# Kernel tuning notes

Measured on AMD Instinct MI355X. Metric: run time of the kernel, lower is better.

Reference implementation:

```python
import jax, jax.numpy as jnp
import numpy as np

LAYER_NUM = 2
NUM_CLS = 128
HIDDEN = 256
NUM_NODES = 1024


def setup_inputs() -> dict:
    key = jax.random.key(0)
    ks = jax.random.split(key, 12)
    s = 0.05
    return {
        "x": jax.random.normal(ks[0], (NUM_NODES, HIDDEN), jnp.float32),
        "knowledge": jax.random.uniform(ks[1], (NUM_CLS, NUM_CLS), jnp.float32) / NUM_CLS,
        "w3w": jax.random.normal(ks[2], (HIDDEN, 2 * HIDDEN), jnp.float32) * s,
        "b3w": jax.random.normal(ks[3], (HIDDEN,), jnp.float32) * s,
        "u3": jax.random.normal(ks[4], (HIDDEN, HIDDEN), jnp.float32) * s,
        "bu3": jax.random.normal(ks[5], (HIDDEN,), jnp.float32) * s,
        "w4w": jax.random.normal(ks[6], (HIDDEN, 2 * HIDDEN), jnp.float32) * s,
        "b4w": jax.random.normal(ks[7], (HIDDEN,), jnp.float32) * s,
        "w5w": jax.random.normal(ks[8], (HIDDEN, 2 * HIDDEN), jnp.float32) * s,
        "b5w": jax.random.normal(ks[9], (HIDDEN,), jnp.float32) * s,
        "u5": jax.random.normal(ks[10], (HIDDEN, HIDDEN), jnp.float32) * s,
        "bu5": jax.random.normal(ks[11], (HIDDEN,), jnp.float32) * s,
    }


def reference(x, knowledge, w3w, b3w, u3, bu3, w4w, b4w, w5w, b5w, u5, bu5):
    N, H = x.shape
    C = knowledge.shape[0]
    # hidden[n, c, :] = x[n, :]  (repeat per class)
    hidden = jnp.broadcast_to(x[:, None, :], (N, C, H))
    for _ in range(LAYER_NUM):
        hs = hidden.sum(0)                      # [C, H]
        diff = hs[None, :, :] - hidden          # [N, C, H]
        # knowledge.T @ diff_n  and  knowledge @ diff_n, vectorized over nodes
        left = jnp.einsum('kc,nkh->nch', knowledge, diff)
        right = jnp.einsum('ck,nkh->nch', knowledge, diff)
        av = jnp.concatenate([left, right], axis=-1).reshape(N * C, 2 * H)
        h = hidden.reshape(N * C, H)
        uh3 = h @ u3.T + bu3                    # shared: rv uses fc_eq3_u (source quirk)
        zv = jax.nn.sigmoid(av @ w3w.T + b3w + uh3)
        rv = jax.nn.sigmoid(av @ w4w.T + b4w + uh3)
        hv = jnp.tanh(av @ w5w.T + b5w + (rv * h) @ u5.T + bu5)
        h = (1.0 - zv) * h + zv * hv
        hidden = h.reshape(N, C, H)
    return hidden
```

## Files before the change

kernel.cpp:

```cpp
#include <hip/hip_runtime.h>
#include <cstdint>
#include <cstddef>


#define NODES 1024
#define NCLS  128
#define HID   256

using frag  = __attribute__((ext_vector_type(8))) short;
using frag4 = __attribute__((ext_vector_type(4))) short;
using f32x4 = __attribute__((ext_vector_type(4))) float;

__device__ __forceinline__ float bf2f(unsigned short h){
  unsigned int u = ((unsigned int)h) << 16;
  float f; __builtin_memcpy(&f, &u, 4); return f;
}
__device__ __forceinline__ unsigned short f2bf(float f){
  unsigned int u; __builtin_memcpy(&u, &f, 4);
  u = (u + 0x7fffu + ((u >> 16) & 1u)) >> 16;
  return (unsigned short)u;
}
__device__ __forceinline__ float sigm(float x){ return 1.0f/(1.0f + __expf(-x)); }
__device__ __forceinline__ float tanh_fast(float x){ return 1.0f - 2.0f/(__expf(2.0f*x) + 1.0f); }

#define GLOBAL_AS(p) ((const __attribute__((address_space(1))) void*)(p))
#define LDS_AS(p)    ((__attribute__((address_space(3))) void*)(p))
#define MFMA16 __builtin_amdgcn_mfma_f32_16x16x32_bf16

template<int OUT_BF16>
__global__ __launch_bounds__(256) void gemm_bf16(
    const unsigned short* __restrict__ A0, int ldA0, int K0,
    const unsigned short* __restrict__ A1, int ldA1,
    const unsigned short* __restrict__ BT, int ldB, long bStride,
    void* __restrict__ Cptr, int ldC,
    int Ntiles, int Ktot, unsigned int aMask, int Mtiles)
{
  __shared__ unsigned short As[4096];
  __shared__ unsigned short Bs[4096];
  const int t   = threadIdx.x;
  const int bid = blockIdx.x;
  const int xcd = bid & 7, slot = bid >> 3;
  const int mtPerX = (Mtiles >= 8) ? (Mtiles >> 3) : 1;
  const int mt = xcd * mtPerX + slot / Ntiles;
  const int nt = slot % Ntiles;
  const int lane = t & 63, w = t >> 6;
  const int wm = w >> 1, wn = w & 1;
  const int r = lane & 15, q = lane >> 4;
  const int m0 = mt * 128, n0 = nt * 128;
  const unsigned short* Bbase = BT + (size_t)mt * (size_t)bStride;

  f32x4 acc[4][4] = {};

  for (int kb = 0; kb < Ktot; kb += 32) {
#pragma unroll
    for (int i = 0; i < 2; ++i) {
      int u  = i * 256 + t;
      int mi = u >> 2;
      int kc = (u & 3) * 8;
      int k  = kb + kc;
      const unsigned short* ga;
      if (k < K0) ga = A0 + (size_t)((unsigned int)(m0 + mi) & aMask) * (size_t)ldA0 + k;
      else        ga = A1 + (size_t)(m0 + mi) * (size_t)ldA1 + (k - K0);
      __builtin_amdgcn_global_load_lds(GLOBAL_AS(ga), LDS_AS(&As[u * 8]), 16, 0, 0);
      const unsigned short* gb = Bbase + (size_t)(n0 + mi) * (size_t)ldB + k;
      __builtin_amdgcn_global_load_lds(GLOBAL_AS(gb), LDS_AS(&Bs[u * 8]), 16, 0, 0);
    }
    __syncthreads();

    frag af[4], bf_[4];
#pragma unroll
    for (int x = 0; x < 4; ++x) {
      af[x]  = *(const frag*)&As[(wm * 64 + x * 16 + r) * 32 + q * 8];
      bf_[x] = *(const frag*)&Bs[(wn * 64 + x * 16 + r) * 32 + q * 8];
    }
#pragma unroll
    for (int x = 0; x < 4; ++x)
#pragma unroll
      for (int y = 0; y < 4; ++y)
        acc[x][y] = MFMA16(af[x], bf_[y], acc[x][y], 0, 0, 0);
    __syncthreads();
  }

#pragma unroll
  for (int x = 0; x < 4; ++x) {
#pragma unroll
    for (int y = 0; y < 4; ++y) {
      int col = n0 + wn * 64 + y * 16 + r;
#pragma unroll
      for (int g = 0; g < 4; ++g) {
        long row = m0 + wm * 64 + x * 16 + q * 4 + g;
        if (OUT_BF16) ((unsigned short*)Cptr)[row * (long)ldC + col] = f2bf(acc[x][y][g]);
        else          ((float*)Cptr)[row * (long)ldC + col] = acc[x][y][g];
      }
    }
  }
}

__global__ __launch_bounds__(512, 2) void gemm_pre(
    const unsigned short* __restrict__ AVH, const unsigned short* __restrict__ H1,
    const unsigned short* __restrict__ WB, const float* __restrict__ SG,
    unsigned short* __restrict__ PRE)
{
  __shared__ __align__(16) unsigned short SM[65536];
  const int t   = threadIdx.x;
  const int bid = blockIdx.x;
  const int xcd = bid & 7, slot = bid >> 3;
  const int mt = xcd * 64 + slot / 3;
  const int ct = slot % 3;
  const int lane = t & 63, w = t >> 6;
  const int wm = w >> 2, wn = w & 3;
  const int r = lane & 15, q = lane >> 4;
  const int m0 = mt * 256;
  const unsigned short* Wrow = WB + (size_t)(ct * 256) * 768;
  const int nkt = (ct < 2) ? 12 : 8;

  unsigned short* const Ab0 = SM;
  unsigned short* const Ab1 = SM + 16384;
  unsigned short* const Bb0 = SM + 32768;
  unsigned short* const Bb1 = SM + 49152;

  f32x4 acc[8][4] = {};

  const int smi = t >> 3, sc = t & 7;

  auto ISSUE_A = [&](unsigned short* dst, int kt, int rbase) {
    int row = rbase + smi;
    int gc = sc ^ (row & 7);
    const unsigned short* ga;
    if (kt < 8) ga = AVH + (size_t)(m0 + row) * 512 + kt * 64 + gc * 8;
    else        ga = H1  + (size_t)(m0 + row) * 256 + (kt - 8) * 64 + gc * 8;
    __builtin_amdgcn_global_load_lds(GLOBAL_AS(ga), LDS_AS(&dst[row * 64 + sc * 8]), 16, 0, 0);
  };
  auto ISSUE_B = [&](unsigned short* dst, int kt, int rbase) {
    int row = rbase + smi;
    int gc = sc ^ (row & 7);
    __builtin_amdgcn_global_load_lds(GLOBAL_AS(Wrow + (size_t)row * 768 + kt * 64 + gc * 8),
                                     LDS_AS(&dst[row * 64 + sc * 8]), 16, 0, 0);
  };

  ISSUE_B(Bb0, 0, 0); ISSUE_B(Bb0, 0, 64); ISSUE_B(Bb0, 0, 128); ISSUE_B(Bb0, 0, 192);
  ISSUE_A(Ab0, 0, 0); ISSUE_A(Ab0, 0, 128); ISSUE_A(Ab0, 0, 64); ISSUE_A(Ab0, 0, 192);
  asm volatile("s_waitcnt vmcnt(2)" ::: "memory");
  __builtin_amdgcn_s_barrier();

#define PRE_PHASE(XG0, ISSUES, TAIL)                                         \
    {                                                                        \
      int ra0 = wm * 128 + (XG0) * 16 + r, ra1 = ra0 + 16;                   \
      frag a00 = *(const frag*)&A[ra0 * 64 + ((q ^ (ra0 & 7)) * 8)];         \
      frag a01 = *(const frag*)&A[ra0 * 64 + (((4 + q) ^ (ra0 & 7)) * 8)];   \
      frag a10 = *(const frag*)&A[ra1 * 64 + ((q ^ (ra1 & 7)) * 8)];         \
      frag a11 = *(const frag*)&A[ra1 * 64 + (((4 + q) ^ (ra1 & 7)) * 8)];   \
      ISSUES;                                                                \
      __builtin_amdgcn_s_setprio(1);                                         \
      _Pragma("unroll")                                                      \
      for (int y = 0; y < 4; ++y) {                                          \
        acc[(XG0)][y]     = MFMA16(a00, bf[y][0], acc[(XG0)][y], 0, 0, 0);   \
        acc[(XG0)][y]     = MFMA16(a01, bf[y][1], acc[(XG0)][y], 0, 0, 0);   \
        acc[(XG0)+1][y]   = MFMA16(a10, bf[y][0], acc[(XG0)+1][y], 0, 0, 0); \
        acc[(XG0)+1][y]   = MFMA16(a11, bf[y][1], acc[(XG0)+1][y], 0, 0, 0); \
      }                                                                      \
      __builtin_amdgcn_s_setprio(0);                                         \
      TAIL;                                                                  \
      asm volatile("" ::: "memory");                                         \
      __builtin_amdgcn_s_barrier();                                          \
    }

  for (int kt = 0; kt < nkt; ++kt) {
    unsigned short* A  = (kt & 1) ? Ab1 : Ab0;
    unsigned short* B  = (kt & 1) ? Bb1 : Bb0;
    unsigned short* An = (kt & 1) ? Ab0 : Ab1;
    unsigned short* Bn = (kt & 1) ? Bb0 : Bb1;
    const bool more = (kt + 1 < nkt);

    frag bf[4][2];
#pragma unroll
    for (int y = 0; y < 4; ++y) {
      int rb = wn * 64 + y * 16 + r;
      bf[y][0] = *(const frag*)&B[rb * 64 + ((q ^ (rb & 7)) * 8)];
      bf[y][1] = *(const frag*)&B[rb * 64 + (((4 + q) ^ (rb & 7)) * 8)];
    }

    PRE_PHASE(0,
      { if (more) { ISSUE_B(Bn, kt + 1, 0); ISSUE_B(Bn, kt + 1, 64); } },
      { })
    PRE_PHASE(2,
      { if (more) { ISSUE_B(Bn, kt + 1, 128); ISSUE_B(Bn, kt + 1, 192); } },
      { if (more) asm volatile("s_waitcnt vmcnt(4)" ::: "memory");
        else      asm volatile("s_waitcnt vmcnt(0)" ::: "memory"); })
    PRE_PHASE(4,
      { if (more) { ISSUE_A(An, kt + 1, 0); ISSUE_A(An, kt + 1, 128); } },
      { })
    PRE_PHASE(6,
      { if (more) { ISSUE_A(An, kt + 1, 64); ISSUE_A(An, kt + 1, 192); } },
      { if (more) asm volatile("s_waitcnt vmcnt(2)" ::: "memory"); })
  }
#undef PRE_PHASE

  unsigned short* L = SM;
#pragma unroll
  for (int xg = 0; xg < 8; ++xg) {
#pragma unroll
    for (int y = 0; y < 4; ++y) {
      int j = wn * 64 + y * 16 + r;
      int jc = j >> 3, jl = j & 7;
#pragma unroll
      for (int g = 0; g < 4; ++g) {
        int c = wm * 128 + xg * 16 + q * 4 + g;
        L[c * 256 + ((jc ^ (c & 31)) * 8) + jl] = f2bf(acc[xg][y][g]);
      }
    }
  }
  __syncthreads();
  if (ct == 1) {
#pragma unroll
    for (int rr = 0; rr < 16; ++rr) {
      int unit = rr * 512 + t;
      int row = unit >> 5, ch = unit & 31;
      size_t grow = (size_t)(m0 + row);
      frag v  = *(const frag*)&L[row * 256 + ((ch ^ (row & 31)) * 8)];
      frag hh = *(const frag*)(H1 + grow * 256 + ch * 8);
      const float* sgr = SG + (size_t)(row & 127) * 768 + 256 + ch * 8;
      f32x4 s0 = *(const f32x4*)(sgr);
      f32x4 s1 = *(const f32x4*)(sgr + 4);
      frag o;
#pragma unroll
      for (int e = 0; e < 8; ++e) {
        float sv = (e < 4) ? s0[e] : s1[e - 4];
        float rv = sigm(sv + bf2f((unsigned short)v[e]));
        o[e] = (short)f2bf(rv * bf2f((unsigned short)hh[e]));
      }
      *(frag*)&PRE[grow * 768 + 256 + ch * 8] = o;
    }
  } else {
#pragma unroll
    for (int rr = 0; rr < 16; ++rr) {
      int unit = rr * 512 + t;
      int row = unit >> 5, ch = unit & 31;
      frag v = *(const frag*)&L[row * 256 + ((ch ^ (row & 31)) * 8)];
      *(frag*)&PRE[(size_t)(m0 + row) * 768 + ct * 256 + ch * 8] = v;
    }
  }
}

__global__ __launch_bounds__(256, 2) void gemm_l1(
    const float* __restrict__ XW, const float* __restrict__ SW,
    const float* __restrict__ x,
    const float* __restrict__ b3, const float* __restrict__ b4,
    const float* __restrict__ b5, const float* __restrict__ bu3,
    const float* __restrict__ bu5,
    const float* __restrict__ colsum, const float* __restrict__ rowsum,
    const unsigned short* __restrict__ u5b,
    const unsigned short* __restrict__ KTbN, const unsigned short* __restrict__ KbN,
    unsigned short* __restrict__ H1, unsigned short* __restrict__ AVH)
{
  __shared__ unsigned short SM[17408];
  unsigned short* As = SM;
  unsigned short* Bs = SM + 4096;
  unsigned short* L  = SM;
  __shared__ float tP1[256], tP2[256], tP3[256], tX[256];
  __shared__ float tZ1[256], tZ2[256], tZ3[256];
  __shared__ float tV1[256], tV2[256], tV3[256];
  __shared__ float tCS[128], tRS[128];

  const int t = threadIdx.x, bid = blockIdx.x;
  const int xcd = bid & 7, slot = bid >> 3;
  const int n  = xcd * 128 + (slot >> 1);
  const int nt = slot & 1;
  const int lane = t & 63, w = t >> 6, wm = w >> 1, wn = w & 1;
  const int r = lane & 15, q = lane >> 4;
  const int n0 = nt * 128;
  const float* xw = XW + (size_t)n * 1792;

  {
    int i = t;
    float xwi0 = xw[i], xwi1 = xw[256 + i], xwi2 = xw[512 + i], xwi3 = xw[768 + i];
    float xwi4 = xw[1024 + i], xwi5 = xw[1280 + i], xwu = xw[1536 + i];
    tP1[i] = SW[512 + i] - xwi2;
    tP2[i] = SW[768 + i] - xwi3;
    tP3[i] = xwu + b4[i] + bu3[i];
    tX[i]  = x[(size_t)n * HID + i];
    tZ1[i] = SW[i] - xwi0;
    tZ2[i] = SW[256 + i] - xwi1;
    tZ3[i] = xwu + b3[i] + bu3[i];
    tV1[i] = SW[1024 + i] - xwi4;
    tV2[i] = SW[1280 + i] - xwi5;
    tV3[i] = b5[i] + bu5[i];
    if (t < 128) { tCS[t] = colsum[t]; tRS[t] = rowsum[t]; }
  }
  __syncthreads();

  f32x4 acc[4][4] = {};

  for (int kb = 0; kb < 256; kb += 32) {
#pragma unroll
    for (int i = 0; i < 2; ++i) {
      int u  = i * 256 + t;
      int mi = u >> 2;
      int c  = u & 3;
      int k  = kb + c * 8;
      int gc = c ^ ((mi >> 1) & 3);
      __builtin_amdgcn_global_load_lds(GLOBAL_AS(u5b + (size_t)(n0 + mi) * 256 + kb + gc * 8),
                                       LDS_AS(&Bs[u * 8]), 16, 0, 0);
      float cs = tCS[mi], rs = tRS[mi];
      frag a;
#pragma unroll
      for (int e = 0; e < 8; ++e) {
        int i2 = k + e;
        float pre = cs * tP1[i2] + rs * tP2[i2] + tP3[i2];
        a[e] = (short)f2bf(sigm(pre) * tX[i2]);
      }
      *(frag*)&As[mi * 32 + (gc * 8)] = a;
    }
    __syncthreads();

    frag af[4], bf_[4];
#pragma unroll
    for (int xx = 0; xx < 4; ++xx) {
      int ra = wm * 64 + xx * 16 + r;
      int rb = wn * 64 + xx * 16 + r;
      af[xx]  = *(const frag*)&As[ra * 32 + ((q ^ ((ra >> 1) & 3)) * 8)];
      bf_[xx] = *(const frag*)&Bs[rb * 32 + ((q ^ ((rb >> 1) & 3)) * 8)];
    }
#pragma unroll
    for (int xx = 0; xx < 4; ++xx)
#pragma unroll
      for (int y = 0; y < 4; ++y)
        acc[xx][y] = MFMA16(af[xx], bf_[y], acc[xx][y], 0, 0, 0);
    __syncthreads();
  }

#pragma unroll
  for (int xx = 0; xx < 4; ++xx) {
#pragma unroll
    for (int y = 0; y < 4; ++y) {
      int j = wn * 64 + y * 16 + r;
      int i = n0 + j;
      frag4 pack;
#pragma unroll
      for (int g = 0; g < 4; ++g) {
        int c = wm * 64 + xx * 16 + q * 4 + g;
        float cs = tCS[c], rs = tRS[c];
        float z  = sigm(cs * tZ1[i] + rs * tZ2[i] + tZ3[i]);
        float p5 = cs * tV1[i] + rs * tV2[i] + tV3[i] + acc[xx][y][g];
        float h1 = (1.0f - z) * tX[i] + z * tanh_fast(p5);
        unsigned short hb = f2bf(h1);
        pack[g] = (short)hb;
        H1[(size_t)(n * 128 + c) * HID + i] = hb;
      }
      *(frag4*)&L[j * 136 + (wm * 64 + xx * 16 + q * 4)] = pack;
    }
  }
  __syncthreads();

#pragma unroll 1
  for (int s = 0; s < 2; ++s) {
    const unsigned short* Ks = s ? KbN : KTbN;
#pragma unroll
    for (int xx = 0; xx < 4; ++xx)
#pragma unroll
      for (int y = 0; y < 4; ++y)
        acc[xx][y] = (f32x4){0.0f, 0.0f, 0.0f, 0.0f};
#pragma unroll
    for (int kb = 0; kb < 4; ++kb) {
      frag af[4], bf_[4];
#pragma unroll
      for (int xx = 0; xx < 4; ++xx) {
        int cp = wm * 64 + xx * 16 + r;
        af[xx] = *(const frag*)(Ks + (size_t)cp * 128 + kb * 32 + q * 8);
        int j = wn * 64 + xx * 16 + r;
        bf_[xx] = *(const frag*)&L[j * 136 + kb * 32 + q * 8];
      }
#pragma unroll
      for (int xx = 0; xx < 4; ++xx)
#pragma unroll
        for (int y = 0; y < 4; ++y)
          acc[xx][y] = MFMA16(af[xx], bf_[y], acc[xx][y], 0, 0, 0);
    }
#pragma unroll
    for (int xx = 0; xx < 4; ++xx)
#pragma unroll
      for (int y = 0; y < 4; ++y) {
        int col = s * 256 + n0 + wn * 64 + y * 16 + r;
#pragma unroll
        for (int g = 0; g < 4; ++g) {
          int cp = wm * 64 + xx * 16 + q * 4 + g;
          AVH[(size_t)(n * 128 + cp) * 512 + col] = f2bf(acc[xx][y][g]);
        }
      }
  }
}

__global__ __launch_bounds__(256, 3) void gemm_l2(
    const unsigned short* __restrict__ PRE, const float* __restrict__ SG,
    const unsigned short* __restrict__ H1, const unsigned short* __restrict__ u5b,
    float* __restrict__ out)
{
  __shared__ __align__(16) unsigned short SM[16384];
  unsigned short* const As = SM;
  unsigned short* const Bs = SM + 4096;
  float* L = (float*)SM;

  const int t = threadIdx.x, bid = blockIdx.x;
  const int xcd = bid & 7, slot = bid >> 3;
  const int mt = xcd * 128 + (slot >> 1);
  const int nt = slot & 1;
  const int lane = t & 63, w = t >> 6, wm = w >> 1, wn = w & 1;
  const int r = lane & 15, q = lane >> 4;
  const int m0 = mt * 128, n0 = nt * 128;

  f32x4 acc[4][4] = {};

  for (int kb = 0; kb < 256; kb += 32) {
#pragma unroll
    for (int i = 0; i < 2; ++i) {
      int u  = i * 256 + t;
      int mi = u >> 2;
      int gc = (u & 3) ^ ((mi >> 1) & 3);
      __builtin_amdgcn_global_load_lds(GLOBAL_AS(PRE + (size_t)(m0 + mi) * 768 + 256 + kb + gc * 8),
                                       LDS_AS(&As[u * 8]), 16, 0, 0);
      __builtin_amdgcn_global_load_lds(GLOBAL_AS(u5b + (size_t)(n0 + mi) * 256 + kb + gc * 8),
                                       LDS_AS(&Bs[u * 8]), 16, 0, 0);
    }
    __syncthreads();

    frag af[4], bf_[4];
#pragma unroll
    for (int xx = 0; xx < 4; ++xx) {
      int ra = wm * 64 + xx * 16 + r;
      int rb = wn * 64 + xx * 16 + r;
      af[xx]  = *(const frag*)&As[ra * 32 + ((q ^ ((ra >> 1) & 3)) * 8)];
      bf_[xx] = *(const frag*)&Bs[rb * 32 + ((q ^ ((rb >> 1) & 3)) * 8)];
    }
#pragma unroll
    for (int xx = 0; xx < 4; ++xx)
#pragma unroll
      for (int y = 0; y < 4; ++y)
        acc[xx][y] = MFMA16(af[xx], bf_[y], acc[xx][y], 0, 0, 0);
    __syncthreads();
  }

  const int lr_r = t >> 2;
  const int cb   = t & 3;
#pragma unroll 1
  for (int p = 0; p < 2; ++p) {
    if (p) __syncthreads();
    if (wm == p) {
#pragma unroll
      for (int xx = 0; xx < 4; ++xx)
#pragma unroll
        for (int y = 0; y < 4; ++y) {
          int j = wn * 64 + y * 16 + r;
#pragma unroll
          for (int g = 0; g < 4; ++g) {
            int lr = xx * 16 + q * 4 + g;
            L[lr * 128 + (j ^ ((lr & 7) << 2))] = acc[xx][y][g];
          }
        }
    }
    __syncthreads();
    long grow = m0 + p * 64 + lr_r;
    int cc = (int)(grow & 127);
    const unsigned short* prow = PRE + (size_t)grow * 768;
    const unsigned short* hrow = H1 + (size_t)grow * 256;
    const float* sgr = SG + (size_t)cc * 768;
    const int off = (lr_r & 7) << 2;
#pragma unroll
    for (int gi = 0; gi < 4; ++gi) {
      int j0 = cb * 8 + gi * 32;
      int i0 = n0 + j0;
      f32x4 a0 = *(const f32x4*)&L[lr_r * 128 + (j0 ^ off)];
      f32x4 a1 = *(const f32x4*)&L[lr_r * 128 + ((j0 + 4) ^ off)];
      frag pz = *(const frag*)(prow + i0);
      frag pp = *(const frag*)(prow + 512 + i0);
      frag hh = *(const frag*)(hrow + i0);
      f32x4 sz0 = *(const f32x4*)(sgr + i0);
      f32x4 sz1 = *(const f32x4*)(sgr + i0 + 4);
      f32x4 sp0 = *(const f32x4*)(sgr + 512 + i0);
      f32x4 sp1 = *(const f32x4*)(sgr + 512 + i0 + 4);
      f32x4 o0, o1;
#pragma unroll
      for (int e = 0; e < 8; ++e) {
        float sz = (e < 4) ? sz0[e] : sz1[e - 4];
        float sp = (e < 4) ? sp0[e] : sp1[e - 4];
        float av = (e < 4) ? a0[e] : a1[e - 4];
        float z  = sigm(sz + bf2f((unsigned short)pz[e]));
        float pv = sp + bf2f((unsigned short)pp[e]) + av;
        float h  = bf2f((unsigned short)hh[e]);
        float o  = (1.0f - z) * h + z * tanh_fast(pv);
        if (e < 4) o0[e] = o; else o1[e - 4] = o;
      }
      *(f32x4*)&out[(size_t)grow * 256 + i0] = o0;
      *(f32x4*)&out[(size_t)grow * 256 + i0 + 4] = o1;
    }
  }
}

__global__ __launch_bounds__(256) void prep_cast(
    const float* __restrict__ x, const float* __restrict__ Kn,
    const float* __restrict__ w3, const float* __restrict__ u3,
    const float* __restrict__ w4, const float* __restrict__ w5,
    const float* __restrict__ u5,
    unsigned short* __restrict__ xb, unsigned short* __restrict__ WB,
    unsigned short* __restrict__ WB2, unsigned short* __restrict__ u5b,
    unsigned short* __restrict__ KbN, unsigned short* __restrict__ KTbN)
{
  int idx = blockIdx.x * 256 + threadIdx.x;
  if (idx < 262144) { xb[idx] = f2bf(x[idx]); return; }
  idx -= 262144;
  if (idx < 589824) {
    int col = idx / 768, j = idx % 768;
    int g = col >> 8, i = col & 255;
    float v;
    if (j < 512) { const float* wg = (g == 0) ? w3 : (g == 1) ? w4 : w5; v = wg[(size_t)i * 512 + j]; }
    else v = (g < 2) ? u3[(size_t)i * 256 + (j - 512)] : 0.0f;
    WB[(size_t)col * 768 + j] = f2bf(v);
    return;
  }
  idx -= 589824;
  if (idx < 458752) {
    int col = idx / 256, h = idx % 256;
    int b = col >> 8, i = col & 255;
    float v = (b < 6) ? ((b < 2 ? w3 : (b < 4 ? w4 : w5))[(size_t)i * 512 + (b & 1) * 256 + h])
                      : u3[(size_t)i * 256 + h];
    WB2[(size_t)col * 256 + h] = f2bf(v);
    return;
  }
  idx -= 458752;
  if (idx < 65536) { u5b[idx] = f2bf(u5[idx]); return; }
  idx -= 65536;
  if (idx < 16384) { int c = idx >> 7, k = idx & 127; KbN[idx]  = f2bf(-Kn[c * 128 + k]); return; }
  idx -= 16384;
  { int c = idx >> 7, k = idx & 127; KTbN[idx] = f2bf(-Kn[k * 128 + c]); }
}

__global__ __launch_bounds__(256) void prep_reduce(
    const float* __restrict__ x, const float* __restrict__ Kn,
    float* __restrict__ S, float* __restrict__ colsum, float* __restrict__ rowsum)
{
  int b = blockIdx.x, t = threadIdx.x;
  if (b < 8) {
    float s = 0.f;
    for (int n = 0; n < 128; ++n) s += x[(size_t)(b * 128 + n) * HID + t];
    atomicAdd(&S[t], s);
  } else if (b == 8) {
    if (t < NCLS) { float s = 0.f; for (int k = 0; k < NCLS; ++k) s += Kn[k * NCLS + t]; colsum[t] = s; }
  } else {
    if (t < NCLS) { float s = 0.f; for (int k = 0; k < NCLS; ++k) s += Kn[t * NCLS + k]; rowsum[t] = s; }
  }
}

__global__ __launch_bounds__(256) void prep_sw(
    const float* __restrict__ S, const float* __restrict__ w3,
    const float* __restrict__ w4, const float* __restrict__ w5, float* __restrict__ SW)
{
  int col = blockIdx.x * 256 + threadIdx.x;
  int b = col >> 8, i = col & 255;
  const float* w = (b < 2) ? w3 : (b < 4) ? w4 : w5;
  const float* row = w + (size_t)i * 512 + (b & 1) * 256;
  float s = 0.f;
  for (int h = 0; h < HID; ++h) s += S[h] * row[h];
  SW[col] = s;
}

__global__ __launch_bounds__(256) void reduce_hs(
    const unsigned short* __restrict__ H1, float* __restrict__ hs)
{
  int bid = blockIdx.x;
  int c = bid >> 5, nch = bid & 31;
  int i = threadIdx.x;
  const unsigned short* p = H1 + (size_t)nch * 32 * NCLS * HID + (size_t)c * HID + i;
  float s = 0.f;
  for (int n = 0; n < 32; ++n) s += bf2f(p[(size_t)n * NCLS * HID]);
  atomicAdd(&hs[c * HID + i], s);
}

__global__ __launch_bounds__(256) void p2a(
    const float* __restrict__ hs, const float* __restrict__ w3,
    const float* __restrict__ w4, const float* __restrict__ w5, float* __restrict__ hsW)
{
  __shared__ float hrow[HID];
  int k = blockIdx.x & 127, b = blockIdx.x >> 7;
  int t = threadIdx.x;
  hrow[t] = hs[k * HID + t];
  __syncthreads();
  const float* w = (b < 2) ? w3 : (b < 4) ? w4 : w5;
  const float* row = w + (size_t)t * 512 + (b & 1) * 256;
  float s = 0.f;
  for (int h = 0; h < HID; ++h) s += hrow[h] * row[h];
  hsW[(size_t)k * 1536 + b * 256 + t] = s;
}

__global__ __launch_bounds__(256) void p2b(
    const float* __restrict__ hsW, const float* __restrict__ Kn,
    const float* __restrict__ b3, const float* __restrict__ b4, const float* __restrict__ b5,
    const float* __restrict__ bu3, const float* __restrict__ bu5, float* __restrict__ SG)
{
  __shared__ float kc[NCLS], kr[NCLS];
  int c = blockIdx.x, t = threadIdx.x;
  if (t < NCLS) { kc[t] = Kn[t * NCLS + c]; kr[t] = Kn[c * NCLS + t]; }
  __syncthreads();
  for (int g = 0; g < 3; ++g) {
    int i = t;
    const float* L = hsW + (size_t)(2 * g) * 256 + i;
    const float* R = hsW + (size_t)(2 * g + 1) * 256 + i;
    float s = 0.f;
    for (int k = 0; k < NCLS; ++k) s += kc[k] * L[(size_t)k * 1536] + kr[k] * R[(size_t)k * 1536];
    const float* bg = (g == 0) ? b3 : (g == 1) ? b4 : b5;
    s += bg[i] + ((g < 2) ? bu3[i] : bu5[i]);
    SG[(size_t)c * 768 + g * 256 + i] = s;
  }
}

extern "C" void kernel_launch(void* const* d_in, const int* in_sizes, int n_in,
                              void* d_out, int out_size, void* d_ws, size_t ws_size,
                              hipStream_t stream) {
  (void)in_sizes; (void)n_in; (void)out_size; (void)ws_size;
  const float* x   = (const float*)d_in[0];
  const float* Kn  = (const float*)d_in[1];
  const float* w3  = (const float*)d_in[2];
  const float* b3  = (const float*)d_in[3];
  const float* u3  = (const float*)d_in[4];
  const float* bu3 = (const float*)d_in[5];
  const float* w4  = (const float*)d_in[6];
  const float* b4  = (const float*)d_in[7];
  const float* w5  = (const float*)d_in[8];
  const float* b5  = (const float*)d_in[9];
  const float* u5  = (const float*)d_in[10];
  const float* bu5 = (const float*)d_in[11];
  float* out = (float*)d_out;

  char* w = (char*)d_ws;
  unsigned short* AVH = (unsigned short*)(w);
  unsigned short* PRE = (unsigned short*)(w + 134217728);
  unsigned short* H1  = (unsigned short*)(w + 335544320);
  float*          XW  = (float*)(w + 402653184);
  char* misc = w + 409993216;
  float* S      = (float*)(misc);
  float* hs     = (float*)(misc + 1024);
  float* SW     = (float*)(misc + 132096);
  float* colsum = (float*)(misc + 138240);
  float* rowsum = (float*)(misc + 138752);
  float* hsW    = (float*)(misc + 139264);
  float* SG     = (float*)(misc + 925696);
  unsigned short* WB   = (unsigned short*)(misc + 1318912);
  unsigned short* WB2  = (unsigned short*)(misc + 2498560);
  unsigned short* u5b  = (unsigned short*)(misc + 3416064);
  unsigned short* KbN  = (unsigned short*)(misc + 3547136);
  unsigned short* KTbN = (unsigned short*)(misc + 3579904);
  unsigned short* xb   = (unsigned short*)(misc + 3612672);

  hipMemsetAsync(misc, 0, 132096, stream);

  prep_cast<<<5504, 256, 0, stream>>>(x, Kn, w3, u3, w4, w5, u5, xb, WB, WB2, u5b, KbN, KTbN);
  prep_reduce<<<10, 256, 0, stream>>>(x, Kn, S, colsum, rowsum);
  prep_sw<<<6, 256, 0, stream>>>(S, w3, w4, w5, SW);

  gemm_bf16<0><<<8 * 14, 256, 0, stream>>>(xb, 256, 256, xb, 256, WB2, 256, 0L,
                                           (void*)XW, 1792, 14, 256, 0xFFFFFFFFu, 8);
  gemm_l1<<<2048, 256, 0, stream>>>(XW, SW, x, b3, b4, b5, bu3, bu5,
                                    colsum, rowsum, u5b, KTbN, KbN, H1, AVH);

  reduce_hs<<<4096, 256, 0, stream>>>(H1, hs);
  p2a<<<768, 256, 0, stream>>>(hs, w3, w4, w5, hsW);
  p2b<<<128, 256, 0, stream>>>(hsW, Kn, b3, b4, b5, bu3, bu5, SG);

  gemm_pre<<<1536, 512, 0, stream>>>(AVH, H1, WB, SG, PRE);

  gemm_l2<<<2048, 256, 0, stream>>>(PRE, SG, H1, u5b, out);
}
```

Baseline: 686.3 us.

## Double-buffer A/B tiles in gemm_l1 to overlap staging with MFMA

Converts the gemm_l1 main K-loop to double-buffered shared-memory tiles. The next u5 B tile is issued via global_load_lds and the next sigmoid-gated A tile is computed while the current tile's MFMAs run, which removes one barrier per iteration. The cost is twice the LDS footprint within the existing SM array and more live registers, which may hurt occupancy at launch bounds of 2.

```diff
diff --git a/kernel.cpp b/kernel.cpp
--- a/kernel.cpp
+++ b/kernel.cpp
@@ -254,8 +254,6 @@
     unsigned short* __restrict__ H1, unsigned short* __restrict__ AVH)
 {
   __shared__ unsigned short SM[17408];
-  unsigned short* As = SM;
-  unsigned short* Bs = SM + 4096;
   unsigned short* L  = SM;
   __shared__ float tP1[256], tP2[256], tP3[256], tX[256];
   __shared__ float tZ1[256], tZ2[256], tZ3[256];
@@ -289,9 +287,7 @@
   }
   __syncthreads();
 
-  f32x4 acc[4][4] = {};
-
-  for (int kb = 0; kb < 256; kb += 32) {
+  auto PREP_A = [&](unsigned short* Asb, int kb) {
 #pragma unroll
     for (int i = 0; i < 2; ++i) {
       int u  = i * 256 + t;
@@ -299,8 +295,6 @@
       int c  = u & 3;
       int k  = kb + c * 8;
       int gc = c ^ ((mi >> 1) & 3);
-      __builtin_amdgcn_global_load_lds(GLOBAL_AS(u5b + (size_t)(n0 + mi) * 256 + kb + gc * 8),
-                                       LDS_AS(&Bs[u * 8]), 16, 0, 0);
       float cs = tCS[mi], rs = tRS[mi];
       frag a;
 #pragma unroll
@@ -309,18 +303,46 @@
         float pre = cs * tP1[i2] + rs * tP2[i2] + tP3[i2];
         a[e] = (short)f2bf(sigm(pre) * tX[i2]);
       }
-      *(frag*)&As[mi * 32 + (gc * 8)] = a;
-    }
-    __syncthreads();
+      *(frag*)&Asb[mi * 32 + (gc * 8)] = a;
+    }
+  };
+  auto STAGE_B = [&](unsigned short* Bsb, int kb) {
+#pragma unroll
+    for (int i = 0; i < 2; ++i) {
+      int u  = i * 256 + t;
+      int mi = u >> 2;
+      int c  = u & 3;
+      int gc = c ^ ((mi >> 1) & 3);
+      __builtin_amdgcn_global_load_lds(GLOBAL_AS(u5b + (size_t)(n0 + mi) * 256 + kb + gc * 8),
+                                       LDS_AS(&Bsb[u * 8]), 16, 0, 0);
+    }
+  };
+
+  PREP_A(SM, 0);
+  STAGE_B(SM + 8192, 0);
+  __syncthreads();
+
+  f32x4 acc[4][4] = {};
+
+  for (int kb = 0; kb < 256; kb += 32) {
+    const int cur = (kb >> 5) & 1;
+    const unsigned short* Asb = SM + cur * 4096;
+    const unsigned short* Bsb = SM + 8192 + cur * 4096;
 
     frag af[4], bf_[4];
 #pragma unroll
     for (int xx = 0; xx < 4; ++xx) {
       int ra = wm * 64 + xx * 16 + r;
       int rb = wn * 64 + xx * 16 + r;
-      af[xx]  = *(const frag*)&As[ra * 32 + ((q ^ ((ra >> 1) & 3)) * 8)];
-      bf_[xx] = *(const frag*)&Bs[rb * 32 + ((q ^ ((rb >> 1) & 3)) * 8)];
-    }
+      af[xx]  = *(const frag*)&Asb[ra * 32 + ((q ^ ((ra >> 1) & 3)) * 8)];
+      bf_[xx] = *(const frag*)&Bsb[rb * 32 + ((q ^ ((rb >> 1) & 3)) * 8)];
+    }
+
+    if (kb < 224) {
+      STAGE_B(SM + 8192 + (cur ^ 1) * 4096, kb + 32);
+      PREP_A(SM + (cur ^ 1) * 4096, kb + 32);
+    }
+
 #pragma unroll
     for (int xx = 0; xx < 4; ++xx)
 #pragma unroll
```

New measurement: 677.5 us, median of 2. About the same (-1.3%).
